# Kernel tuning notes

Measured on AMD Instinct MI355X. Metric: run time of the kernel, lower is better.

Reference implementation:

```python
import jax, jax.numpy as jnp
import numpy as np
from jax import lax


def setup_inputs() -> dict:
    key = jax.random.key(0)
    ks = jax.random.split(key, 10)
    B, T, Din, U = 64, 256, 128, 1024
    def rn(k, shape, sc=0.02):
        return jax.random.normal(k, shape, jnp.float32) * sc
    return {
        "inputs": jax.random.normal(ks[0], (B, T, Din), jnp.float32),
        "We1": rn(ks[1], (Din, U)), "be1": jnp.zeros((U,), jnp.float32),
        "We2": rn(ks[2], (U, U)),   "be2": jnp.zeros((U,), jnp.float32),
        "W1": rn(ks[3], (U, U)),    "b1": jnp.zeros((U,), jnp.float32),
        "W2": rn(ks[4], (U, U)),    "b2": jnp.zeros((U,), jnp.float32),
        "V": rn(ks[5], (U, 1)),     "bV": jnp.zeros((1,), jnp.float32),
        "Wk": rn(ks[6], (U, 4 * U)),
        "Wr": rn(ks[7], (U, 4 * U)),
        "bl": jnp.zeros((4 * U,), jnp.float32),
        "Wo": rn(ks[8], (U, 1)),    "bo": jnp.zeros((1,), jnp.float32),
        "seq_len": 256,
    }


def reference(inputs, We1, be1, We2, be2, W1, b1, W2, b2, V, bV,
              Wk, Wr, bl, Wo, bo, seq_len):
    B = inputs.shape[0]
    U = Wr.shape[0]
    f32 = inputs.dtype
    # Frozen embedding ANN, applied per timestep: [B,T,Din] -> [B,T,U]
    h1 = jax.nn.relu(inputs @ We1 + be1)
    x = jax.nn.relu(h1 @ We2 + be2)            # attention values [B,T,U]
    # W2(values) is constant across decode steps; hoist out of the loop.
    keys = x @ W2 + b2                          # [B,T,U]

    def step(carry, _):
        h, c = carry                            # [B,U] each
        # Bahdanau attention: score = V(tanh(W1(q) + W2(values)))
        q = h @ W1 + b1                         # [B,U]
        score = jnp.tanh(q[:, None, :] + keys) @ V + bV   # [B,T,1]
        attw = jax.nn.softmax(score, axis=1)    # softmax over time axis
        ctx = jnp.sum(attw * x, axis=1)         # context vector [B,U]
        # Keras LSTM cell (gate order i,f,g,o; sigmoid recurrent, tanh act)
        z = ctx @ Wk + h @ Wr + bl              # [B,4U]
        i, f, g, o = jnp.split(z, 4, axis=-1)
        i = jax.nn.sigmoid(i)
        f = jax.nn.sigmoid(f)
        g = jnp.tanh(g)
        o = jax.nn.sigmoid(o)
        c_new = f * c + i * g
        h_new = o * jnp.tanh(c_new)
        out = h_new @ Wo + bo                   # [B,1]
        return (h_new, c_new), out

    init = (jnp.zeros((B, U), f32), jnp.zeros((B, U), f32))
    _, outs = lax.scan(step, init, None, length=seq_len)   # [seq_len,B,1]
    return jnp.squeeze(outs, axis=2)            # [seq_len, B]
```

## Files before the change

kernel.cpp:

```cpp
#include <hip/hip_runtime.h>

#define U_ 1024
#define B_ 64
#define T_ 256
#define DIN_ 128
#define BT_ (B_*T_)
#define G_ 1024
#define NWB 576

#define FA_L   0
#define RELA_L 64
#define CE_L   128
#define CZ_L   192
#define CX_L   208
#define RELX_L 272
#define CC_L   336
#define RELC_L 352
#define SYNC_N (416*16)

typedef __attribute__((ext_vector_type(4))) float f32x4;
typedef __attribute__((ext_vector_type(8))) short s16x8;
typedef __attribute__((ext_vector_type(4))) unsigned short u16x4;
typedef unsigned long long u64;

union U64F2 { u64 q; float f[2]; };
union U64H4 { u64 q; unsigned short h[4]; };

__device__ inline unsigned short f2bf(float x){
  unsigned u = __float_as_uint(x);
  u += 0x7FFFu + ((u >> 16) & 1u);
  return (unsigned short)(u >> 16);
}
__device__ inline float bf2f(unsigned short b){ return __uint_as_float(((unsigned)b) << 16); }
__device__ inline float fast_rcp(float x){ return __builtin_amdgcn_rcpf(x); }
__device__ inline float fast_tanh(float x){
  float e = __expf(2.0f * x);
  return 1.0f - 2.0f * fast_rcp(e + 1.0f);
}
__device__ inline float fast_sig(float x){
  return fast_rcp(1.0f + __expf(-x));
}

__device__ inline u64 ald64(const u64* p){
  return __hip_atomic_load((u64*)p, __ATOMIC_RELAXED, __HIP_MEMORY_SCOPE_AGENT);
}
__device__ inline void ast64(u64* p, u64 v){
  __hip_atomic_store(p, v, __ATOMIC_RELAXED, __HIP_MEMORY_SCOPE_AGENT);
}
__device__ inline float aldf(const float* p){
  return __hip_atomic_load((float*)p, __ATOMIC_RELAXED, __HIP_MEMORY_SCOPE_AGENT);
}
__device__ inline void astf(float* p, float v){
  __hip_atomic_store(p, v, __ATOMIC_RELAXED, __HIP_MEMORY_SCOPE_AGENT);
}
__device__ inline unsigned ald32(const unsigned* p){
  return __hip_atomic_load((unsigned*)p, __ATOMIC_RELAXED, __HIP_MEMORY_SCOPE_AGENT);
}
__device__ inline void ast32(unsigned* p, unsigned v){
  __hip_atomic_store(p, v, __ATOMIC_RELAXED, __HIP_MEMORY_SCOPE_AGENT);
}
__device__ inline void aadd32(unsigned* p, unsigned v){
  __hip_atomic_fetch_add(p, v, __ATOMIC_RELAXED, __HIP_MEMORY_SCOPE_AGENT);
}
__device__ inline s16x8 frag_ald(const u64* p){
  u64 a = ald64(p), b = ald64(p + 1);
  union { u64 q[2]; s16x8 v; } x; x.q[0] = a; x.q[1] = b; return x.v;
}
__device__ inline s16x8 bc16(f32x4 v){ return __builtin_bit_cast(s16x8, v); }

__device__ inline void wait1(unsigned* line, unsigned tgt){
  if (threadIdx.x == 0){
    while (ald32(line) < tgt) __builtin_amdgcn_s_sleep(2);
  }
  __syncthreads();
}

__device__ inline void wait1_acq(unsigned* line, unsigned tgt){
  if (threadIdx.x == 0){
    while (ald32(line) < tgt) __builtin_amdgcn_s_sleep(2);
    __builtin_amdgcn_fence(__ATOMIC_ACQUIRE, "agent");
  }
  __syncthreads();
}

__device__ inline f32x4 bcast_gemm_sc0(const char* gp, const unsigned short* lfrag,
                                       int lane){
  f32x4 acc = (f32x4){0.f,0.f,0.f,0.f};
  #pragma unroll
  for (int ii = 0; ii < 4; ++ii){
    const char* g = gp + ii*512;
    f32x4 t0,t1,t2,t3,t4,t5,t6,t7;
    asm volatile("global_load_dwordx4 %0, %1, off sc0"            : "=v"(t0) : "v"(g));
    asm volatile("global_load_dwordx4 %0, %1, off offset:64 sc0"  : "=v"(t1) : "v"(g));
    asm volatile("global_load_dwordx4 %0, %1, off offset:128 sc0" : "=v"(t2) : "v"(g));
    asm volatile("global_load_dwordx4 %0, %1, off offset:192 sc0" : "=v"(t3) : "v"(g));
    asm volatile("global_load_dwordx4 %0, %1, off offset:256 sc0" : "=v"(t4) : "v"(g));
    asm volatile("global_load_dwordx4 %0, %1, off offset:320 sc0" : "=v"(t5) : "v"(g));
    asm volatile("global_load_dwordx4 %0, %1, off offset:384 sc0" : "=v"(t6) : "v"(g));
    asm volatile("global_load_dwordx4 %0, %1, off offset:448 sc0" : "=v"(t7) : "v"(g));
    asm volatile("s_waitcnt vmcnt(0)" ::: "memory");
    __builtin_amdgcn_sched_barrier(0);
    const unsigned short* lb = lfrag + (size_t)ii*8*512 + lane*8;
    acc = __builtin_amdgcn_mfma_f32_16x16x32_bf16(bc16(t0), *(const s16x8*)(lb + 0*512), acc, 0, 0, 0);
    acc = __builtin_amdgcn_mfma_f32_16x16x32_bf16(bc16(t1), *(const s16x8*)(lb + 1*512), acc, 0, 0, 0);
    acc = __builtin_amdgcn_mfma_f32_16x16x32_bf16(bc16(t2), *(const s16x8*)(lb + 2*512), acc, 0, 0, 0);
    acc = __builtin_amdgcn_mfma_f32_16x16x32_bf16(bc16(t3), *(const s16x8*)(lb + 3*512), acc, 0, 0, 0);
    acc = __builtin_amdgcn_mfma_f32_16x16x32_bf16(bc16(t4), *(const s16x8*)(lb + 4*512), acc, 0, 0, 0);
    acc = __builtin_amdgcn_mfma_f32_16x16x32_bf16(bc16(t5), *(const s16x8*)(lb + 5*512), acc, 0, 0, 0);
    acc = __builtin_amdgcn_mfma_f32_16x16x32_bf16(bc16(t6), *(const s16x8*)(lb + 6*512), acc, 0, 0, 0);
    acc = __builtin_amdgcn_mfma_f32_16x16x32_bf16(bc16(t7), *(const s16x8*)(lb + 7*512), acc, 0, 0, 0);
  }
  return acc;
}

__device__ inline float score8(s16x8 k0, s16x8 k1, const float* tqv, const float* Vv){
  float s = 0.f;
  #pragma unroll
  for (int e = 0; e < 8; ++e){
    float kf = bf2f((unsigned short)k0[e]);
    float num = tqv[e] + kf;
    float den = fmaf(tqv[e], kf, 1.0f);
    s += Vv[e] * num * fast_rcp(den);
  }
  #pragma unroll
  for (int e = 0; e < 8; ++e){
    float kf = bf2f((unsigned short)k1[e]);
    float num = tqv[8+e] + kf;
    float den = fmaf(tqv[8+e], kf, 1.0f);
    s += Vv[8+e] * num * fast_rcp(den);
  }
  return s;
}

__global__ void init_kernel(float* c, unsigned short* hb0, unsigned short* hb1,
                            unsigned* sync, const float* V, float* vbound){
  int i = blockIdx.x * 256 + threadIdx.x;
  if (i < B_*U_){ c[i] = 0.f; hb0[i] = 0; hb1[i] = 0; }
  if (i < SYNC_N) sync[i] = 0u;
  if (blockIdx.x == 0){
    __shared__ float red[4];
    int t = threadIdx.x, lane = t & 63, w = t >> 6;
    float s = fabsf(V[t]) + fabsf(V[t+256]) + fabsf(V[t+512]) + fabsf(V[t+768]);
    #pragma unroll
    for (int mk = 32; mk >= 1; mk >>= 1) s += __shfl_xor(s, mk, 64);
    if (lane == 0) red[w] = s;
    __syncthreads();
    if (t == 0) vbound[0] = red[0] + red[1] + red[2] + red[3];
  }
}

__global__ void transpose_bf_kernel(const float* W, unsigned short* WT, int K, int N){
  int ktiles = K >> 5;
  int kb = blockIdx.x % ktiles, nb = blockIdx.x / ktiles;
  __shared__ float tile[32][33];
  int x = threadIdx.x & 31, y8 = threadIdx.x >> 5;
  #pragma unroll
  for (int i = 0; i < 4; ++i){
    int y = y8*4 + i;
    tile[y][x] = W[(size_t)(kb*32 + y)*N + nb*32 + x];
  }
  __syncthreads();
  #pragma unroll
  for (int i = 0; i < 4; ++i){
    int y = y8*4 + i;
    WT[(size_t)(nb*32 + y)*K + kb*32 + x] = f2bf(tile[x][y]);
  }
}

template<int AF32>
__global__ __launch_bounds__(256) void gemm_embed(const void* Aptr, const unsigned short* BT,
                                                  const float* bias, unsigned short* Cout,
                                                  int K, int act){
  int nb = blockIdx.x & 15, mb = blockIdx.x >> 4;
  int lane = threadIdx.x & 63, w = threadIdx.x >> 6;
  int l15 = lane & 15, quad = lane >> 4;
  int m0 = mb*64 + w*16;
  int arow = m0 + l15;
  f32x4 acc[4];
  #pragma unroll
  for (int nt = 0; nt < 4; ++nt) acc[nt] = (f32x4){0.f,0.f,0.f,0.f};

  for (int k0 = 0; k0 < K; k0 += 32){
    int koff = k0 + quad*8;
    s16x8 a8;
    if (AF32){
      const float* ap = (const float*)Aptr + (size_t)arow*K + koff;
      f32x4 lo = *(const f32x4*)ap;
      f32x4 hi = *(const f32x4*)(ap + 4);
      a8[0]=(short)f2bf(lo[0]); a8[1]=(short)f2bf(lo[1]); a8[2]=(short)f2bf(lo[2]); a8[3]=(short)f2bf(lo[3]);
      a8[4]=(short)f2bf(hi[0]); a8[5]=(short)f2bf(hi[1]); a8[6]=(short)f2bf(hi[2]); a8[7]=(short)f2bf(hi[3]);
    } else {
      a8 = *(const s16x8*)((const unsigned short*)Aptr + (size_t)arow*K + koff);
    }
    #pragma unroll
    for (int nt = 0; nt < 4; ++nt){
      const unsigned short* bp = BT + (size_t)(nb*64 + nt*16 + l15)*K + koff;
      s16x8 b8 = *(const s16x8*)bp;
      acc[nt] = __builtin_amdgcn_mfma_f32_16x16x32_bf16(a8, b8, acc[nt], 0, 0, 0);
    }
  }
  #pragma unroll
  for (int nt = 0; nt < 4; ++nt){
    int col = nb*64 + nt*16 + l15;
    float bv = bias[col];
    #pragma unroll
    for (int r = 0; r < 4; ++r){
      int row = m0 + quad*4 + r;
      float v = acc[nt][r] + bv;
      v = (act == 0) ? fmaxf(v, 0.f) : fast_tanh(v);
      Cout[(size_t)row*U_ + col] = f2bf(v);
    }
  }
}

struct SeqP {
  const unsigned short *W1Tb, *WkTb, *WrTb, *tk, *xv;
  const float *b1, *bl, *V, *Wo, *bo, *vbound;
  float *tq, *ew, *c, *zh, *out_part, *out;
  unsigned short *ctxb, *hb0, *hb1;
  unsigned *sync;
};

__device__ inline void out_reduce(const SeqP& p, int b, int sidx, float* smem,
                                  int t, int lane, int w){
  float v = aldf(&p.out_part[b*256 + t]);
  #pragma unroll
  for (int mk = 32; mk >= 1; mk >>= 1) v += __shfl_xor(v, mk, 64);
  if (lane == 0) smem[w] = v;
  __syncthreads();
  if (t == 0) astf(&p.out[sidx*64 + b], smem[0] + smem[1] + smem[2] + smem[3] + p.bo[0]);
  __syncthreads();
}

__global__ __launch_bounds__(256, 4) void seq_kernel(SeqP p){
  const int bi = blockIdx.x;
  const int t  = threadIdx.x;
  const int lane = t & 63, w = t >> 6;
  const int l15 = lane & 15, quad = lane >> 4;
  __shared__ __align__(16) unsigned short lfrag[16384];
  __shared__ __align__(16) float smem[1664];
  unsigned* sync = p.sync;
  const float Mb = p.vbound[0];

  if (bi < NWB){
    const unsigned short* wsrc;
    if (bi < 64)       wsrc = p.W1Tb + (size_t)(bi*16 + l15)*U_;
    else if (bi < 320) wsrc = p.WrTb + (size_t)((bi - 64)*16 + l15)*U_;
    else               wsrc = p.WkTb + (size_t)((l15 >> 2)*U_ + (bi - 320)*4 + (l15 & 3))*U_;
    for (int it = w; it < 32; it += 4)
      *(s16x8*)&lfrag[it*512 + lane*8] = *(const s16x8*)(wsrc + it*32 + quad*8);
  } else {
    const unsigned short* xsrc = p.xv + (size_t)(bi >> 4)*T_*U_ + (bi & 15)*64;
    #pragma unroll
    for (int it = 0; it < 8; ++it){
      int r = (t >> 3) + 32*it;
      *(s16x8*)&lfrag[r*64 + (t & 7)*8] = *(const s16x8*)(xsrc + (size_t)r*U_ + (t & 7)*8);
    }
  }
  __syncthreads();

  u64* tqu  = (u64*)p.tq;
  u64* ewu  = (u64*)p.ew;
  u64* zhu  = (u64*)p.zh;
  u64* ctxu = (u64*)p.ctxb;

  for (int step = 0; step < T_; ++step){
    const u64* hbRu = (const u64*)((step & 1) ? p.hb1 : p.hb0);
    u64*       hbWu = (u64*)((step & 1) ? p.hb0 : p.hb1);

    if (bi < 64){
      wait1_acq(&sync[(RELC_L + (bi & 63))*16], (unsigned)step);
      int jcol = bi*16 + l15;
      const char* hp = (const char*)hbRu + (size_t)(w*16 + l15)*2048 + quad*16;
      f32x4 acc = bcast_gemm_sc0(hp, lfrag, lane);
      float bj = p.b1[jcol];
      float* tqs = smem;
      #pragma unroll
      for (int r = 0; r < 4; ++r)
        tqs[l15*68 + w*16 + quad*4 + r] = fast_tanh(acc[r] + bj);
      __syncthreads();
      if (t < 64){
        int ub64 = (t*U_ + bi*16) >> 1;
        #pragma unroll
        for (int cc = 0; cc < 16; cc += 2){
          U64F2 x;
          x.f[0] = tqs[(cc+0)*68 + t];
          x.f[1] = tqs[(cc+1)*68 + t];
          ast64(tqu + ub64 + (cc >> 1), x.q);
        }
      }
      __syncthreads();
      if (t == 0) ast32(&sync[(FA_L + bi)*16], (unsigned)(step + 1));
      if (bi == 0){
        if (t < 64){
          unsigned tgt = (unsigned)(step + 1);
          for (;;){
            bool ok = ald32(&sync[(FA_L + t)*16]) >= tgt;
            if (__ballot(ok) == ~0ull) break;
            __builtin_amdgcn_s_sleep(1);
          }
          ast32(&sync[(RELA_L + t)*16], tgt);
        }
      }
    } else if (bi < 320){
      wait1_acq(&sync[(RELC_L + (bi & 63))*16], (unsigned)step);
      int bz = bi - 64;
      int jc0 = bz*16 + l15;
      const char* hp = (const char*)hbRu + (size_t)(w*16 + l15)*2048 + quad*16;
      f32x4 acc0 = bcast_gemm_sc0(hp, lfrag, lane);
      float bl0 = p.bl[jc0];
      int brow = w*16 + quad*4;
      U64F2 x;
      int i0 = (jc0*64 + brow) >> 1;
      x.f[0] = acc0[0] + bl0; x.f[1] = acc0[1] + bl0; ast64(zhu + i0, x.q);
      x.f[0] = acc0[2] + bl0; x.f[1] = acc0[3] + bl0; ast64(zhu + i0 + 1, x.q);
      __syncthreads();
      if (t == 0) aadd32(&sync[(CZ_L + ((bi - 64) & 15))*16], 1u);
    } else if (bi >= 960){
      if (bi == 960){
        if (step > 0){
          if (t < 64){
            unsigned tgt = 16u * (unsigned)step;
            for (;;){
              bool ok = (t < 16) ? (ald32(&sync[(CC_L + t)*16]) >= tgt) : true;
              if (__ballot(ok) == ~0ull) break;
              __builtin_amdgcn_s_sleep(1);
            }
            ast32(&sync[(RELC_L + t)*16], (unsigned)step);
          }
          __syncthreads();
          out_reduce(p, 0, step - 1, smem, t, lane, w);
        }
      } else {
        wait1(&sync[(RELC_L + (bi & 63))*16], (unsigned)step);
        if (step > 0) out_reduce(p, bi - 960, step - 1, smem, t, lane, w);
      }
    }

    wait1(&sync[(RELA_L + (bi & 63))*16], (unsigned)(step + 1));
    {
      int b = bi >> 4, tg = bi & 15;
      float tqv[16], Vv[16];
      int tqb = (b*U_ + lane*16) >> 1;
      #pragma unroll
      for (int i = 0; i < 8; ++i){
        U64F2 x; x.q = ald64(tqu + tqb + i);
        tqv[2*i] = x.f[0]; tqv[2*i+1] = x.f[1];
      }
      const float* Vp = p.V + lane*16;
      #pragma unroll
      for (int i = 0; i < 16; i += 4) *(f32x4*)&Vv[i] = *(const f32x4*)(Vp + i);
      int trow = tg*16 + w*4;
      float sr[4];
      const unsigned short* kp = p.tk + (size_t)(b*T_ + trow)*U_ + lane*16;
      #pragma unroll
      for (int rr = 0; rr < 4; ++rr){
        s16x8 k0 = *(const s16x8*)(kp + (size_t)rr*U_);
        s16x8 k1 = *(const s16x8*)(kp + (size_t)rr*U_ + 8);
        sr[rr] = score8(k0, k1, tqv, Vv);
      }
      #pragma unroll
      for (int mk = 32; mk >= 1; mk >>= 1){
        #pragma unroll
        for (int rr = 0; rr < 4; ++rr) sr[rr] += __shfl_xor(sr[rr], mk, 64);
      }
      if (lane == 0){
        int eb = (b*T_ + trow) >> 1;
        #pragma unroll
        for (int j = 0; j < 2; ++j){
          U64F2 x;
          x.f[0] = __expf(sr[2*j]   - Mb);
          x.f[1] = __expf(sr[2*j+1] - Mb);
          ast64(ewu + eb + j, x.q);
        }
      }
    }
    __syncthreads();
    if (t == 0) aadd32(&sync[(CE_L + (bi >> 4))*16], 1u);

    wait1(&sync[(CE_L + (bi >> 4))*16], 16u * (unsigned)(step + 1));
    {
      int b = bi >> 4, ug = bi & 15;
      float* ewL = smem;
      float* tmp = smem + 256;
      float* red = smem + 272;
      if (t < 128){
        U64F2 x; x.q = ald64(ewu + b*128 + t);
        ewL[2*t] = x.f[0]; ewL[2*t+1] = x.f[1];
      }
      __syncthreads();
      float e = ewL[t];
      float sum = e;
      #pragma unroll
      for (int mk = 32; mk >= 1; mk >>= 1) sum += __shfl_xor(sum, mk, 64);
      if (lane == 0) tmp[w] = sum;
      __syncthreads();
      float rd = fast_rcp(tmp[0] + tmp[1] + tmp[2] + tmp[3]);

      int ui = t & 15, tgp = t >> 4;
      f32x4 a = (f32x4){0.f,0.f,0.f,0.f};
      if (bi >= NWB){
        #pragma unroll 4
        for (int t8 = tgp; t8 < T_; t8 += 16){
          float wg = ewL[t8];
          u16x4 x4 = *(const u16x4*)&lfrag[t8*64 + ui*4];
          a[0] = fmaf(wg, bf2f(x4[0]), a[0]);
          a[1] = fmaf(wg, bf2f(x4[1]), a[1]);
          a[2] = fmaf(wg, bf2f(x4[2]), a[2]);
          a[3] = fmaf(wg, bf2f(x4[3]), a[3]);
        }
      } else {
        int u = ug*64 + ui*4;
        const unsigned short* xp = p.xv + (size_t)b*T_*U_ + u;
        #pragma unroll 4
        for (int t8 = tgp; t8 < T_; t8 += 16){
          float wg = ewL[t8];
          u16x4 x4 = *(const u16x4*)(xp + (size_t)t8*U_);
          a[0] = fmaf(wg, bf2f(x4[0]), a[0]);
          a[1] = fmaf(wg, bf2f(x4[1]), a[1]);
          a[2] = fmaf(wg, bf2f(x4[2]), a[2]);
          a[3] = fmaf(wg, bf2f(x4[3]), a[3]);
        }
      }
      *(f32x4*)&red[(tgp*16 + ui)*4] = a;
      __syncthreads();
      if (t < 16){
        f32x4 r = (f32x4){0.f,0.f,0.f,0.f};
        #pragma unroll
        for (int g = 0; g < 16; ++g){
          f32x4 rr = *(f32x4*)&red[(g*16 + t)*4];
          r[0]+=rr[0]; r[1]+=rr[1]; r[2]+=rr[2]; r[3]+=rr[3];
        }
        U64H4 cv;
        cv.h[0]=f2bf(r[0]*rd); cv.h[1]=f2bf(r[1]*rd); cv.h[2]=f2bf(r[2]*rd); cv.h[3]=f2bf(r[3]*rd);
        ast64(ctxu + b*256 + ug*16 + t, cv.q);
      }
    }
    __syncthreads();
    if (t == 0) aadd32(&sync[(CX_L + (bi & 63))*16], 1u);

    if (bi == 576){
      unsigned tgt = 16u * (unsigned)(step + 1);
      if (w == 0){
        for (;;){
          bool ok = ald32(&sync[(CX_L + lane)*16]) >= tgt;
          if (__ballot(ok) == ~0ull) break;
          __builtin_amdgcn_s_sleep(1);
        }
      } else if (w == 1){
        for (;;){
          bool ok = (lane < 16) ? (ald32(&sync[(CZ_L + lane)*16]) >= tgt) : true;
          if (__ballot(ok) == ~0ull) break;
          __builtin_amdgcn_s_sleep(1);
        }
      }
      __syncthreads();
      if (t < 64) ast32(&sync[(RELX_L + t)*16], (unsigned)(step + 1));
    }

    if (bi >= 320 && bi < NWB){
      wait1_acq(&sync[(RELX_L + (bi & 63))*16], (unsigned)(step + 1));
      int cb = bi - 320;
      int ub = cb*4;
      int gate = l15 >> 2, uo = l15 & 3;
      int jcol = gate*U_ + ub + uo;
      const char* cp = (const char*)ctxu + (size_t)(w*16 + l15)*2048 + quad*16;
      f32x4 acc = bcast_gemm_sc0(cp, lfrag, lane);
      int brow = w*16 + quad*4;
      int zi0 = (jcol*64 + brow) >> 1;
      U64F2 z0, z1;
      z0.q = ald64(zhu + zi0); z1.q = ald64(zhu + zi0 + 1);
      acc[0] += z0.f[0]; acc[1] += z0.f[1]; acc[2] += z1.f[0]; acc[3] += z1.f[1];
      float* zs = smem;
      float* hs = smem + 1088;
      float* op = smem + 1344;
      *(f32x4*)&zs[l15*68 + brow] = acc;
      __syncthreads();
      {
        int b = t & 63, ui = t >> 6;
        int u = ub + ui;
        float zi = zs[(0*4 + ui)*68 + b];
        float zf = zs[(1*4 + ui)*68 + b];
        float zg = zs[(2*4 + ui)*68 + b];
        float zo = zs[(3*4 + ui)*68 + b];
        float ig = fast_sig(zi), fg = fast_sig(zf);
        float gg = fast_tanh(zg), og = fast_sig(zo);
        float cold = aldf(&p.c[u*64 + b]);
        float cn = fg*cold + ig*gg;
        float hn = og * fast_tanh(cn);
        astf(&p.c[u*64 + b], cn);
        hs[ui*64 + b] = hn;
        op[ui*64 + b] = hn * p.Wo[u];
      }
      __syncthreads();
      if (t < 64){
        U64H4 h0;
        #pragma unroll
        for (int k = 0; k < 4; ++k) h0.h[k] = f2bf(hs[k*64 + t]);
        ast64(hbWu + t*256 + cb, h0.q);
        float po = op[t] + op[64 + t] + op[128 + t] + op[192 + t];
        astf(&p.out_part[t*256 + cb], po);
      }
      __syncthreads();
      if (t == 0) aadd32(&sync[(CC_L + ((bi - 320) & 15))*16], 1u);
    }
  }

  if (bi == 960){
    if (t < 64){
      unsigned tgt = 16u * (unsigned)T_;
      for (;;){
        bool ok = (t < 16) ? (ald32(&sync[(CC_L + t)*16]) >= tgt) : true;
        if (__ballot(ok) == ~0ull) break;
        __builtin_amdgcn_s_sleep(1);
      }
      ast32(&sync[(RELC_L + t)*16], (unsigned)T_);
    }
    __syncthreads();
    out_reduce(p, 0, T_ - 1, smem, t, lane, w);
  } else if (bi > 960){
    wait1(&sync[(RELC_L + (bi & 63))*16], (unsigned)T_);
    out_reduce(p, bi - 960, T_ - 1, smem, t, lane, w);
  }
}

extern "C" void kernel_launch(void* const* d_in, const int* in_sizes, int n_in,
                              void* d_out, int out_size, void* d_ws, size_t ws_size,
                              hipStream_t stream){
  const float* inputs = (const float*)d_in[0];
  const float* We1 = (const float*)d_in[1];
  const float* be1 = (const float*)d_in[2];
  const float* We2 = (const float*)d_in[3];
  const float* be2 = (const float*)d_in[4];
  const float* W1  = (const float*)d_in[5];
  const float* b1  = (const float*)d_in[6];
  const float* W2  = (const float*)d_in[7];
  const float* b2  = (const float*)d_in[8];
  const float* V   = (const float*)d_in[9];
  const float* Wk  = (const float*)d_in[11];
  const float* Wr  = (const float*)d_in[12];
  const float* bl  = (const float*)d_in[13];
  const float* Wo  = (const float*)d_in[14];
  const float* bo  = (const float*)d_in[15];
  float* out = (float*)d_out;

  char* ws = (char*)d_ws;
  size_t off = 0;
  auto alloc = [&](size_t bytes) -> void* {
    void* pp = ws + off;
    off = (off + bytes + 255) & ~(size_t)255;
    return pp;
  };
  unsigned short* We1Tb = (unsigned short*)alloc((size_t)1024*128*2);
  unsigned short* We2Tb = (unsigned short*)alloc((size_t)1024*1024*2);
  unsigned short* W2Tb  = (unsigned short*)alloc((size_t)1024*1024*2);
  unsigned short* W1Tb  = (unsigned short*)alloc((size_t)1024*1024*2);
  unsigned short* WkTb  = (unsigned short*)alloc((size_t)4096*1024*2);
  unsigned short* WrTb  = (unsigned short*)alloc((size_t)4096*1024*2);
  unsigned short* h1tk  = (unsigned short*)alloc((size_t)BT_*U_*2);
  unsigned short* xv    = (unsigned short*)alloc((size_t)BT_*U_*2);
  float*          c     = (float*)alloc((size_t)B_*U_*4);
  unsigned short* hb0   = (unsigned short*)alloc((size_t)B_*U_*2);
  unsigned short* hb1   = (unsigned short*)alloc((size_t)B_*U_*2);
  unsigned short* ctxb  = (unsigned short*)alloc((size_t)B_*U_*2);
  float*          tq    = (float*)alloc((size_t)B_*U_*4);
  float*          ew    = (float*)alloc((size_t)B_*T_*4);
  float*          zh    = (float*)alloc((size_t)4*U_*64*4);
  float*          out_part = (float*)alloc((size_t)64*256*4);
  unsigned*       sync  = (unsigned*)alloc((size_t)SYNC_N*4);
  float*          vbound= (float*)alloc(256);
  if (ws_size < off) return;

  init_kernel<<<256, 256, 0, stream>>>(c, hb0, hb1, sync, V, vbound);
  transpose_bf_kernel<<<(128/32)*(1024/32),  256, 0, stream>>>(We1, We1Tb, 128, 1024);
  transpose_bf_kernel<<<(1024/32)*(1024/32), 256, 0, stream>>>(We2, We2Tb, 1024, 1024);
  transpose_bf_kernel<<<(1024/32)*(1024/32), 256, 0, stream>>>(W2,  W2Tb,  1024, 1024);
  transpose_bf_kernel<<<(1024/32)*(1024/32), 256, 0, stream>>>(W1,  W1Tb,  1024, 1024);
  transpose_bf_kernel<<<(1024/32)*(4096/32), 256, 0, stream>>>(Wk,  WkTb,  1024, 4096);
  transpose_bf_kernel<<<(1024/32)*(4096/32), 256, 0, stream>>>(Wr,  WrTb,  1024, 4096);

  gemm_embed<1><<<4096, 256, 0, stream>>>((const void*)inputs, We1Tb, be1, h1tk, DIN_, 0);
  gemm_embed<0><<<4096, 256, 0, stream>>>((const void*)h1tk,   We2Tb, be2, xv,   U_,   0);
  gemm_embed<0><<<4096, 256, 0, stream>>>((const void*)xv,     W2Tb,  b2,  h1tk, U_,   1);

  SeqP sp;
  sp.W1Tb = W1Tb; sp.WkTb = WkTb; sp.WrTb = WrTb; sp.tk = h1tk; sp.xv = xv;
  sp.b1 = b1; sp.bl = bl; sp.V = V; sp.Wo = Wo; sp.bo = bo; sp.vbound = vbound;
  sp.tq = tq; sp.ew = ew; sp.c = c; sp.zh = zh;
  sp.out_part = out_part; sp.out = out;
  sp.ctxb = ctxb; sp.hb0 = hb0; sp.hb1 = hb1; sp.sync = sync;
  seq_kernel<<<dim3(G_), dim3(256), 0, stream>>>(sp);
}
```

Baseline: 11.41 ms.

## Replace exp-broadcast barrier with atomic accumulation of unnormalized context numerator

Drops the per-batch barrier that gathered exp-scores from 16 blocks before computing the softmax context. Each block now computes its 16 timesteps' weighted sum of values and atomically adds it into a double-buffered fp32 numerator and denominator. The LSTM gate GEMM reads the fp32 numerator, scales by the reciprocal denominator and converts to bf16 on the fly. This removes one grid-wide sync stage per step at the cost of many float atomics, reading fp32 instead of bf16 context, and zeroing the alternate buffer each step.

```diff
diff --git a/kernel.cpp b/kernel.cpp
--- a/kernel.cpp
+++ b/kernel.cpp
@@ -10,7 +10,6 @@
 
 #define FA_L   0
 #define RELA_L 64
-#define CE_L   128
 #define CZ_L   192
 #define CX_L   208
 #define RELX_L 272
@@ -62,9 +61,8 @@
 __device__ inline void aadd32(unsigned* p, unsigned v){
   __hip_atomic_fetch_add(p, v, __ATOMIC_RELAXED, __HIP_MEMORY_SCOPE_AGENT);
 }
-__device__ inline s16x8 frag_ald(const u64* p){
-  u64 a = ald64(p), b = ald64(p + 1);
-  union { u64 q[2]; s16x8 v; } x; x.q[0] = a; x.q[1] = b; return x.v;
+__device__ inline void aaddf(float* p, float v){
+  __hip_atomic_fetch_add(p, v, __ATOMIC_RELAXED, __HIP_MEMORY_SCOPE_AGENT);
 }
 __device__ inline s16x8 bc16(f32x4 v){ return __builtin_bit_cast(s16x8, v); }
 
@@ -113,6 +111,41 @@
   return acc;
 }
 
+__device__ inline s16x8 cvt8(f32x4 lo, f32x4 hi, float rdv){
+  s16x8 r;
+  r[0]=(short)f2bf(lo[0]*rdv); r[1]=(short)f2bf(lo[1]*rdv);
+  r[2]=(short)f2bf(lo[2]*rdv); r[3]=(short)f2bf(lo[3]*rdv);
+  r[4]=(short)f2bf(hi[0]*rdv); r[5]=(short)f2bf(hi[1]*rdv);
+  r[6]=(short)f2bf(hi[2]*rdv); r[7]=(short)f2bf(hi[3]*rdv);
+  return r;
+}
+
+__device__ inline f32x4 ctx_gemm_sc0(const char* gp, float rdv,
+                                     const unsigned short* lfrag, int lane){
+  f32x4 acc = (f32x4){0.f,0.f,0.f,0.f};
+  #pragma unroll
+  for (int ii = 0; ii < 8; ++ii){
+    const char* g = gp + ii*512;
+    f32x4 l0,h0,l1,h1,l2,h2,l3,h3;
+    asm volatile("global_load_dwordx4 %0, %1, off sc0"            : "=v"(l0) : "v"(g));
+    asm volatile("global_load_dwordx4 %0, %1, off offset:16 sc0"  : "=v"(h0) : "v"(g));
+    asm volatile("global_load_dwordx4 %0, %1, off offset:128 sc0" : "=v"(l1) : "v"(g));
+    asm volatile("global_load_dwordx4 %0, %1, off offset:144 sc0" : "=v"(h1) : "v"(g));
+    asm volatile("global_load_dwordx4 %0, %1, off offset:256 sc0" : "=v"(l2) : "v"(g));
+    asm volatile("global_load_dwordx4 %0, %1, off offset:272 sc0" : "=v"(h2) : "v"(g));
+    asm volatile("global_load_dwordx4 %0, %1, off offset:384 sc0" : "=v"(l3) : "v"(g));
+    asm volatile("global_load_dwordx4 %0, %1, off offset:400 sc0" : "=v"(h3) : "v"(g));
+    asm volatile("s_waitcnt vmcnt(0)" ::: "memory");
+    __builtin_amdgcn_sched_barrier(0);
+    const unsigned short* lb = lfrag + (size_t)ii*4*512 + lane*8;
+    acc = __builtin_amdgcn_mfma_f32_16x16x32_bf16(cvt8(l0,h0,rdv), *(const s16x8*)(lb + 0*512), acc, 0, 0, 0);
+    acc = __builtin_amdgcn_mfma_f32_16x16x32_bf16(cvt8(l1,h1,rdv), *(const s16x8*)(lb + 1*512), acc, 0, 0, 0);
+    acc = __builtin_amdgcn_mfma_f32_16x16x32_bf16(cvt8(l2,h2,rdv), *(const s16x8*)(lb + 2*512), acc, 0, 0, 0);
+    acc = __builtin_amdgcn_mfma_f32_16x16x32_bf16(cvt8(l3,h3,rdv), *(const s16x8*)(lb + 3*512), acc, 0, 0, 0);
+  }
+  return acc;
+}
+
 __device__ inline float score8(s16x8 k0, s16x8 k1, const float* tqv, const float* Vv){
   float s = 0.f;
   #pragma unroll
@@ -133,10 +166,13 @@
 }
 
 __global__ void init_kernel(float* c, unsigned short* hb0, unsigned short* hb1,
-                            unsigned* sync, const float* V, float* vbound){
+                            unsigned* sync, const float* V, float* vbound,
+                            float* num, float* den){
   int i = blockIdx.x * 256 + threadIdx.x;
   if (i < B_*U_){ c[i] = 0.f; hb0[i] = 0; hb1[i] = 0; }
   if (i < SYNC_N) sync[i] = 0u;
+  num[i] = 0.f; num[i + 65536] = 0.f;
+  if (i < 2*64*16) den[i] = 0.f;
   if (blockIdx.x == 0){
     __shared__ float red[4];
     int t = threadIdx.x, lane = t & 63, w = t >> 6;
@@ -216,8 +252,8 @@
 struct SeqP {
   const unsigned short *W1Tb, *WkTb, *WrTb, *tk, *xv;
   const float *b1, *bl, *V, *Wo, *bo, *vbound;
-  float *tq, *ew, *c, *zh, *out_part, *out;
-  unsigned short *ctxb, *hb0, *hb1;
+  float *tq, *c, *zh, *out_part, *out, *num, *den;
+  unsigned short *hb0, *hb1;
   unsigned *sync;
 };
 
@@ -250,19 +286,16 @@
     for (int it = w; it < 32; it += 4)
       *(s16x8*)&lfrag[it*512 + lane*8] = *(const s16x8*)(wsrc + it*32 + quad*8);
   } else {
-    const unsigned short* xsrc = p.xv + (size_t)(bi >> 4)*T_*U_ + (bi & 15)*64;
-    #pragma unroll
-    for (int it = 0; it < 8; ++it){
-      int r = (t >> 3) + 32*it;
-      *(s16x8*)&lfrag[r*64 + (t & 7)*8] = *(const s16x8*)(xsrc + (size_t)r*U_ + (t & 7)*8);
+    const unsigned short* xsrc = p.xv + (size_t)((bi >> 4)*T_ + (bi & 15)*16)*U_;
+    for (int r = w; r < 16; r += 4){
+      *(s16x8*)&lfrag[r*1024 +       lane*8] = *(const s16x8*)(xsrc + (size_t)r*U_ + lane*8);
+      *(s16x8*)&lfrag[r*1024 + 512 + lane*8] = *(const s16x8*)(xsrc + (size_t)r*U_ + 512 + lane*8);
     }
   }
   __syncthreads();
 
   u64* tqu  = (u64*)p.tq;
-  u64* ewu  = (u64*)p.ew;
   u64* zhu  = (u64*)p.zh;
-  u64* ctxu = (u64*)p.ctxb;
 
   for (int step = 0; step < T_; ++step){
     const u64* hbRu = (const u64*)((step & 1) ? p.hb1 : p.hb0);
@@ -364,76 +397,45 @@
         #pragma unroll
         for (int rr = 0; rr < 4; ++rr) sr[rr] += __shfl_xor(sr[rr], mk, 64);
       }
+      float* ewS = smem;
       if (lane == 0){
-        int eb = (b*T_ + trow) >> 1;
         #pragma unroll
-        for (int j = 0; j < 2; ++j){
-          U64F2 x;
-          x.f[0] = __expf(sr[2*j]   - Mb);
-          x.f[1] = __expf(sr[2*j+1] - Mb);
-          ast64(ewu + eb + j, x.q);
-        }
-      }
-    }
-    __syncthreads();
-    if (t == 0) aadd32(&sync[(CE_L + (bi >> 4))*16], 1u);
-
-    wait1(&sync[(CE_L + (bi >> 4))*16], 16u * (unsigned)(step + 1));
-    {
-      int b = bi >> 4, ug = bi & 15;
-      float* ewL = smem;
-      float* tmp = smem + 256;
-      float* red = smem + 272;
-      if (t < 128){
-        U64F2 x; x.q = ald64(ewu + b*128 + t);
-        ewL[2*t] = x.f[0]; ewL[2*t+1] = x.f[1];
-      }
-      __syncthreads();
-      float e = ewL[t];
-      float sum = e;
-      #pragma unroll
-      for (int mk = 32; mk >= 1; mk >>= 1) sum += __shfl_xor(sum, mk, 64);
-      if (lane == 0) tmp[w] = sum;
-      __syncthreads();
-      float rd = fast_rcp(tmp[0] + tmp[1] + tmp[2] + tmp[3]);
-
-      int ui = t & 15, tgp = t >> 4;
+        for (int rr = 0; rr < 4; ++rr) ewS[w*4 + rr] = __expf(sr[rr] - Mb);
+      }
+      __syncthreads();
       f32x4 a = (f32x4){0.f,0.f,0.f,0.f};
       if (bi >= NWB){
-        #pragma unroll 4
-        for (int t8 = tgp; t8 < T_; t8 += 16){
-          float wg = ewL[t8];
-          u16x4 x4 = *(const u16x4*)&lfrag[t8*64 + ui*4];
+        #pragma unroll
+        for (int t16 = 0; t16 < 16; ++t16){
+          float wg = ewS[t16];
+          u16x4 x4 = *(const u16x4*)&lfrag[t16*1024 + w*256 + lane*4];
           a[0] = fmaf(wg, bf2f(x4[0]), a[0]);
           a[1] = fmaf(wg, bf2f(x4[1]), a[1]);
           a[2] = fmaf(wg, bf2f(x4[2]), a[2]);
           a[3] = fmaf(wg, bf2f(x4[3]), a[3]);
         }
       } else {
-        int u = ug*64 + ui*4;
-        const unsigned short* xp = p.xv + (size_t)b*T_*U_ + u;
-        #pragma unroll 4
-        for (int t8 = tgp; t8 < T_; t8 += 16){
-          float wg = ewL[t8];
-          u16x4 x4 = *(const u16x4*)(xp + (size_t)t8*U_);
+        const unsigned short* xp = p.xv + (size_t)(b*T_ + tg*16)*U_ + w*256 + lane*4;
+        #pragma unroll
+        for (int t16 = 0; t16 < 16; ++t16){
+          float wg = ewS[t16];
+          u16x4 x4 = *(const u16x4*)(xp + (size_t)t16*U_);
           a[0] = fmaf(wg, bf2f(x4[0]), a[0]);
           a[1] = fmaf(wg, bf2f(x4[1]), a[1]);
           a[2] = fmaf(wg, bf2f(x4[2]), a[2]);
           a[3] = fmaf(wg, bf2f(x4[3]), a[3]);
         }
       }
-      *(f32x4*)&red[(tgp*16 + ui)*4] = a;
-      __syncthreads();
-      if (t < 16){
-        f32x4 r = (f32x4){0.f,0.f,0.f,0.f};
+      float* nb = p.num + ((size_t)(step & 1)*B_ + b)*U_ + w*256 + lane*4;
+      aaddf(nb + 0, a[0]);
+      aaddf(nb + 1, a[1]);
+      aaddf(nb + 2, a[2]);
+      aaddf(nb + 3, a[3]);
+      if (t == 0){
+        float ds = 0.f;
         #pragma unroll
-        for (int g = 0; g < 16; ++g){
-          f32x4 rr = *(f32x4*)&red[(g*16 + t)*4];
-          r[0]+=rr[0]; r[1]+=rr[1]; r[2]+=rr[2]; r[3]+=rr[3];
-        }
-        U64H4 cv;
-        cv.h[0]=f2bf(r[0]*rd); cv.h[1]=f2bf(r[1]*rd); cv.h[2]=f2bf(r[2]*rd); cv.h[3]=f2bf(r[3]*rd);
-        ast64(ctxu + b*256 + ug*16 + t, cv.q);
+        for (int i = 0; i < 16; ++i) ds += ewS[i];
+        aaddf(&p.den[((step & 1)*64 + b)*16], ds);
       }
     }
     __syncthreads();
@@ -464,8 +466,10 @@
       int ub = cb*4;
       int gate = l15 >> 2, uo = l15 & 3;
       int jcol = gate*U_ + ub + uo;
-      const char* cp = (const char*)ctxu + (size_t)(w*16 + l15)*2048 + quad*16;
-      f32x4 acc = bcast_gemm_sc0(cp, lfrag, lane);
+      int brow16 = w*16 + l15;
+      float rdv = fast_rcp(aldf(&p.den[((step & 1)*64 + brow16)*16]));
+      const char* np = (const char*)(p.num + ((size_t)(step & 1)*B_ + brow16)*U_) + quad*32;
+      f32x4 acc = ctx_gemm_sc0(np, rdv, lfrag, lane);
       int brow = w*16 + quad*4;
       int zi0 = (jcol*64 + brow) >> 1;
       U64F2 z0, z1;
@@ -493,6 +497,11 @@
         op[ui*64 + b] = hn * p.Wo[u];
       }
       __syncthreads();
+      {
+        float* nz = p.num + ((size_t)((step + 1) & 1)*B_ + (cb >> 2))*U_ + (cb & 3)*256;
+        astf(&nz[t], 0.f);
+        if (cb < 64 && t == 0) astf(&p.den[(((step + 1) & 1)*64 + cb)*16], 0.f);
+      }
       if (t < 64){
         U64H4 h0;
         #pragma unroll
@@ -562,16 +571,16 @@
   float*          c     = (float*)alloc((size_t)B_*U_*4);
   unsigned short* hb0   = (unsigned short*)alloc((size_t)B_*U_*2);
   unsigned short* hb1   = (unsigned short*)alloc((size_t)B_*U_*2);
-  unsigned short* ctxb  = (unsigned short*)alloc((size_t)B_*U_*2);
   float*          tq    = (float*)alloc((size_t)B_*U_*4);
-  float*          ew    = (float*)alloc((size_t)B_*T_*4);
   float*          zh    = (float*)alloc((size_t)4*U_*64*4);
+  float*          num   = (float*)alloc((size_t)2*B_*U_*4);
+  float*          den   = (float*)alloc((size_t)2*64*16*4);
   float*          out_part = (float*)alloc((size_t)64*256*4);
   unsigned*       sync  = (unsigned*)alloc((size_t)SYNC_N*4);
   float*          vbound= (float*)alloc(256);
   if (ws_size < off) return;
 
-  init_kernel<<<256, 256, 0, stream>>>(c, hb0, hb1, sync, V, vbound);
+  init_kernel<<<256, 256, 0, stream>>>(c, hb0, hb1, sync, V, vbound, num, den);
   transpose_bf_kernel<<<(128/32)*(1024/32),  256, 0, stream>>>(We1, We1Tb, 128, 1024);
   transpose_bf_kernel<<<(1024/32)*(1024/32), 256, 0, stream>>>(We2, We2Tb, 1024, 1024);
   transpose_bf_kernel<<<(1024/32)*(1024/32), 256, 0, stream>>>(W2,  W2Tb,  1024, 1024);
@@ -586,8 +595,8 @@
   SeqP sp;
   sp.W1Tb = W1Tb; sp.WkTb = WkTb; sp.WrTb = WrTb; sp.tk = h1tk; sp.xv = xv;
   sp.b1 = b1; sp.bl = bl; sp.V = V; sp.Wo = Wo; sp.bo = bo; sp.vbound = vbound;
-  sp.tq = tq; sp.ew = ew; sp.c = c; sp.zh = zh;
+  sp.tq = tq; sp.c = c; sp.zh = zh; sp.num = num; sp.den = den;
   sp.out_part = out_part; sp.out = out;
-  sp.ctxb = ctxb; sp.hb0 = hb0; sp.hb1 = hb1; sp.sync = sync;
+  sp.hb0 = hb0; sp.hb1 = hb1; sp.sync = sync;
   seq_kernel<<<dim3(G_), dim3(256), 0, stream>>>(sp);
 }
```

New measurement: 14.22 ms. 1.25x slower.
